# Performance work log

Measured on AMD Instinct MI355X. Metric: run time of the kernel, lower is better.

## Reference

```python
import jax, jax.numpy as jnp
import numpy as np

B, S, D = 2, 2048, 1024
H = 16
DK = D // H  # 64

def setup_inputs() -> dict:
    key = jax.random.key(0)
    ks = jax.random.split(key, 7)
    scale = 1.0 / np.sqrt(D)
    return {
        "Query": jax.random.normal(ks[0], (B, S, D), dtype=jnp.float32),
        "Key":   jax.random.normal(ks[1], (B, S, D), dtype=jnp.float32),
        "Value": jax.random.normal(ks[2], (B, S, D), dtype=jnp.float32),
        "Wq": jax.random.normal(ks[3], (D, D), dtype=jnp.float32) * scale,
        "Wk": jax.random.normal(ks[4], (D, D), dtype=jnp.float32) * scale,
        "Wv": jax.random.normal(ks[5], (D, D), dtype=jnp.float32) * scale,
        "Wo": jax.random.normal(ks[6], (D, D), dtype=jnp.float32) * scale,
    }

def reference(Query, Key, Value, Wq, Wk, Wv, Wo):
    b = Query.shape[0]
    # nn.Linear(bias=False): x @ W.T ; reshape to [B, H, S, DK]
    q = (Query @ Wq.T).reshape(b, -1, H, DK).transpose(0, 2, 1, 3)
    k = (Key   @ Wk.T).reshape(b, -1, H, DK).transpose(0, 2, 1, 3)
    v = (Value @ Wv.T).reshape(b, -1, H, DK).transpose(0, 2, 1, 3)
    # full O(S^2) score matrix [B, H, Sq, Sk]
    scores = jnp.einsum("bhqd,bhkd->bhqk", q, k) / jnp.sqrt(jnp.float32(DK))
    # FAITHFUL to source: nn.Softmax(dim=1) normalizes over the HEAD axis
    attn = jax.nn.softmax(scores, axis=1)
    ctx = jnp.einsum("bhqk,bhkd->bhqd", attn, v)  # [B, H, Sq, DK]
    ctx = ctx.transpose(0, 2, 1, 3).reshape(b, -1, H * DK)  # [B, S, D]
    return ctx @ Wo.T
```

## Files before the change

### kernel.cpp

```cpp
#include <hip/hip_runtime.h>
#include <stdint.h>

#define BB   2
#define SS   2048
#define DD   1024
#define HH   16
#define DKK  64
#define MM   (BB*SS)

typedef __attribute__((ext_vector_type(4))) float f32x4;
typedef __attribute__((ext_vector_type(8))) short s16x8;

#define MFMA_B16(a, b, c) __builtin_amdgcn_mfma_f32_16x16x32_bf16((a), (b), (c), 0, 0, 0)

__device__ __forceinline__ ushort f2bf(float f) {
  uint u = __float_as_uint(f);
  u += 0x7FFFu + ((u >> 16) & 1u);
  return (ushort)(u >> 16);
}
__device__ __forceinline__ float bf2f(ushort u) {
  return __uint_as_float((uint)u << 16);
}
#if __has_builtin(__builtin_amdgcn_exp2f)
#define EXP2(x) __builtin_amdgcn_exp2f(x)
#else
#define EXP2(x) exp2f(x)
#endif

__device__ __forceinline__ s16x8 pack8(float4 a, float4 b) {
  union { uint u[4]; s16x8 v; } r;
  asm("v_cvt_pk_bf16_f32 %0, %1, %2" : "=v"(r.u[0]) : "v"(a.x), "v"(a.y));
  asm("v_cvt_pk_bf16_f32 %0, %1, %2" : "=v"(r.u[1]) : "v"(a.z), "v"(a.w));
  asm("v_cvt_pk_bf16_f32 %0, %1, %2" : "=v"(r.u[2]) : "v"(b.x), "v"(b.y));
  asm("v_cvt_pk_bf16_f32 %0, %1, %2" : "=v"(r.u[3]) : "v"(b.z), "v"(b.w));
  return r.v;
}
__device__ __forceinline__ s16x8 cvt8(const float* src) {
  return pack8(*(const float4*)src, *(const float4*)(src + 4));
}

#define QSCALE (0.125f * 1.4426950408889634f)

__global__ void cvt4_kernel(const float* __restrict__ s0, const float* __restrict__ s1,
                            const float* __restrict__ s2, const float* __restrict__ s3,
                            ushort* __restrict__ d0, ushort* __restrict__ d1,
                            ushort* __restrict__ d2, ushort* __restrict__ d3, int n) {
  const int w = blockIdx.y;
  const float*  src = (w == 0) ? s0 : (w == 1) ? s1 : (w == 2) ? s2 : s3;
  ushort*       dst = (w == 0) ? d0 : (w == 1) ? d1 : (w == 2) ? d2 : d3;
  int i = (blockIdx.x * 256 + threadIdx.x) * 8;
  if (i >= n) return;
  *(s16x8*)(dst + i) = cvt8(src + i);
}

__global__ __launch_bounds__(256, 2) void qkv_proj(
    const float* __restrict__ Ia, const float* __restrict__ Ib, const float* __restrict__ Ic,
    const ushort* __restrict__ Wa, const ushort* __restrict__ Wb, const ushort* __restrict__ Wc,
    ushort* __restrict__ Oa, ushort* __restrict__ Ob, ushort* __restrict__ Oc)
{
  __shared__ ushort As[2][128 * 32];
  __shared__ ushort Bs[2][128 * 32];
  const int tid  = threadIdx.x;
  const int lane = tid & 63, wave = tid >> 6;
  const int q = lane & 15, g = lane >> 4;
  const int wr = wave >> 1, wc = wave & 1;
  const int mblk = blockIdx.x * 128, nblk = blockIdx.y * 128;
  const int mode = blockIdx.z;

  const float*  A = (mode == 0) ? Ia : (mode == 1) ? Ib : Ic;
  const ushort* W = (mode == 0) ? Wa : (mode == 1) ? Wb : Wc;

  f32x4 acc[4][4];
  {
    f32x4 z = {0.f, 0.f, 0.f, 0.f};
#pragma unroll
    for (int i = 0; i < 4; ++i)
#pragma unroll
      for (int j = 0; j < 4; ++j) acc[i][j] = z;
  }

  const int r0 = tid >> 2;
  const int e0 = (tid & 3) * 8;
  const size_t arow0 = (size_t)(mblk + r0) * 1024 + e0;
  const size_t arow1 = (size_t)(mblk + r0 + 64) * 1024 + e0;
  const size_t wrow0 = (size_t)(nblk + r0) * 1024 + e0;
  const size_t wrow1 = (size_t)(nblk + r0 + 64) * 1024 + e0;

#pragma unroll
  for (int it = 0; it < 2; ++it) {
    const int row = r0 + it * 64;
    *(s16x8*)&As[0][row * 32 + e0] = cvt8(A + (it ? arow1 : arow0));
    *(s16x8*)&Bs[0][row * 32 + e0] = *(const s16x8*)(W + (it ? wrow1 : wrow0));
  }
  float4 fa0_0, fa0_1, fa1_0, fa1_1;
  s16x8  wg0, wg1;
  {
    const float* p0 = A + arow0 + 32;
    const float* p1 = A + arow1 + 32;
    fa0_0 = *(const float4*)p0;  fa0_1 = *(const float4*)(p0 + 4);
    fa1_0 = *(const float4*)p1;  fa1_1 = *(const float4*)(p1 + 4);
    wg0 = *(const s16x8*)(W + wrow0 + 32);
    wg1 = *(const s16x8*)(W + wrow1 + 32);
  }
  __syncthreads();

  for (int s = 0; s < 32; ++s) {
    const int cur = s & 1;
    float4 na0_0, na0_1, na1_0, na1_1;
    s16x8  nw0, nw1;
    if (s < 30) {
      const int k0 = (s + 2) * 32;
      const float* p0 = A + arow0 + k0;
      const float* p1 = A + arow1 + k0;
      na0_0 = *(const float4*)p0;  na0_1 = *(const float4*)(p0 + 4);
      na1_0 = *(const float4*)p1;  na1_1 = *(const float4*)(p1 + 4);
      nw0 = *(const s16x8*)(W + wrow0 + k0);
      nw1 = *(const s16x8*)(W + wrow1 + k0);
    }
    s16x8 af[4], bf[4];
#pragma unroll
    for (int t = 0; t < 4; ++t) {
      af[t] = *(const s16x8*)&As[cur][(wr * 64 + t * 16 + q) * 32 + g * 8];
      bf[t] = *(const s16x8*)&Bs[cur][(wc * 64 + t * 16 + q) * 32 + g * 8];
    }
#pragma unroll
    for (int mt = 0; mt < 4; ++mt)
#pragma unroll
      for (int nt = 0; nt < 4; ++nt)
        acc[mt][nt] = MFMA_B16(af[mt], bf[nt], acc[mt][nt]);
    if (s < 31) {
      *(s16x8*)&As[cur ^ 1][r0 * 32 + e0]        = pack8(fa0_0, fa0_1);
      *(s16x8*)&As[cur ^ 1][(r0 + 64) * 32 + e0] = pack8(fa1_0, fa1_1);
      *(s16x8*)&Bs[cur ^ 1][r0 * 32 + e0]        = wg0;
      *(s16x8*)&Bs[cur ^ 1][(r0 + 64) * 32 + e0] = wg1;
    }
    if (s < 30) {
      fa0_0 = na0_0; fa0_1 = na0_1; fa1_0 = na1_0; fa1_1 = na1_1;
      wg0 = nw0; wg1 = nw1;
    }
    __syncthreads();
  }

  if (mode == 2) {
    ushort* Vt = Oc;
#pragma unroll
    for (int mt = 0; mt < 4; ++mt)
#pragma unroll
      for (int nt = 0; nt < 4; ++nt) {
        const int s0 = mblk + wr * 64 + mt * 16 + g * 4;
        const int o  = nblk + wc * 64 + nt * 16 + q;
        const int h = o >> 6, dk = o & 63;
        const int b = s0 >> 11, sr = s0 & 2047;
        ushort4 pk;
        pk.x = f2bf(acc[mt][nt][0]); pk.y = f2bf(acc[mt][nt][1]);
        pk.z = f2bf(acc[mt][nt][2]); pk.w = f2bf(acc[mt][nt][3]);
        *(ushort4*)(Vt + ((size_t)((b * 16 + h) * 64 + dk)) * SS + sr) = pk;
      }
  } else {
    const float scale = (mode == 0) ? QSCALE : 1.0f;
    ushort* P = (mode == 0) ? Oa : Ob;
    ushort* wl = &As[0][wave * 1024];
    const int h0 = (nblk + wc * 64) >> 6;
#pragma unroll
    for (int mt = 0; mt < 4; ++mt) {
      const int s0 = mblk + wr * 64 + mt * 16;
      const int b  = s0 >> 11, sr0 = s0 & 2047;
#pragma unroll
      for (int nt = 0; nt < 4; ++nt)
#pragma unroll
        for (int j = 0; j < 4; ++j)
          wl[(g * 4 + j) * 64 + nt * 16 + q] = f2bf(acc[mt][nt][j] * scale);
#pragma unroll
      for (int it = 0; it < 2; ++it) {
        s16x8 v = *(const s16x8*)((char*)wl + it * 1024 + lane * 16);
        const int lr = it * 8 + (lane >> 3);
        const int c  = (lane & 7) * 8;
        *(s16x8*)(P + ((size_t)((b * 16 + h0) * SS) + sr0 + lr) * DKK + c) = v;
      }
    }
  }
}

__global__ __launch_bounds__(256, 2) void o_proj(
    const ushort* __restrict__ A, const ushort* __restrict__ W,
    float* __restrict__ O)
{
  __shared__ ushort As[2][128 * 32];
  __shared__ ushort Bs[2][128 * 32];
  const int tid  = threadIdx.x;
  const int lane = tid & 63, wave = tid >> 6;
  const int q = lane & 15, g = lane >> 4;
  const int wr = wave >> 1, wc = wave & 1;
  const int mblk = blockIdx.x * 128, nblk = blockIdx.y * 128;

  f32x4 acc[4][4];
  {
    f32x4 z = {0.f, 0.f, 0.f, 0.f};
#pragma unroll
    for (int i = 0; i < 4; ++i)
#pragma unroll
      for (int j = 0; j < 4; ++j) acc[i][j] = z;
  }

  const int r0 = tid >> 2;
  const int e0 = (tid & 3) * 8;
  const size_t arow0 = (size_t)(mblk + r0) * 1024 + e0;
  const size_t arow1 = (size_t)(mblk + r0 + 64) * 1024 + e0;
  const size_t wrow0 = (size_t)(nblk + r0) * 1024 + e0;
  const size_t wrow1 = (size_t)(nblk + r0 + 64) * 1024 + e0;

#pragma unroll
  for (int it = 0; it < 2; ++it) {
    const int row = r0 + it * 64;
    *(s16x8*)&As[0][row * 32 + e0] = *(const s16x8*)(A + (it ? arow1 : arow0));
    *(s16x8*)&Bs[0][row * 32 + e0] = *(const s16x8*)(W + (it ? wrow1 : wrow0));
  }
  s16x8 ag0, ag1, wg0, wg1;
  {
    ag0 = *(const s16x8*)(A + arow0 + 32);
    ag1 = *(const s16x8*)(A + arow1 + 32);
    wg0 = *(const s16x8*)(W + wrow0 + 32);
    wg1 = *(const s16x8*)(W + wrow1 + 32);
  }
  __syncthreads();

  for (int s = 0; s < 32; ++s) {
    const int cur = s & 1;
    s16x8 na0, na1, nw0, nw1;
    if (s < 30) {
      const int k0 = (s + 2) * 32;
      na0 = *(const s16x8*)(A + arow0 + k0);
      na1 = *(const s16x8*)(A + arow1 + k0);
      nw0 = *(const s16x8*)(W + wrow0 + k0);
      nw1 = *(const s16x8*)(W + wrow1 + k0);
    }
    s16x8 af[4], bf[4];
#pragma unroll
    for (int t = 0; t < 4; ++t) {
      af[t] = *(const s16x8*)&As[cur][(wr * 64 + t * 16 + q) * 32 + g * 8];
      bf[t] = *(const s16x8*)&Bs[cur][(wc * 64 + t * 16 + q) * 32 + g * 8];
    }
#pragma unroll
    for (int mt = 0; mt < 4; ++mt)
#pragma unroll
      for (int nt = 0; nt < 4; ++nt)
        acc[mt][nt] = MFMA_B16(af[mt], bf[nt], acc[mt][nt]);
    if (s < 31) {
      *(s16x8*)&As[cur ^ 1][r0 * 32 + e0]        = ag0;
      *(s16x8*)&As[cur ^ 1][(r0 + 64) * 32 + e0] = ag1;
      *(s16x8*)&Bs[cur ^ 1][r0 * 32 + e0]        = wg0;
      *(s16x8*)&Bs[cur ^ 1][(r0 + 64) * 32 + e0] = wg1;
    }
    if (s < 30) { ag0 = na0; ag1 = na1; wg0 = nw0; wg1 = nw1; }
    __syncthreads();
  }

#pragma unroll
  for (int mt = 0; mt < 4; ++mt)
#pragma unroll
    for (int nt = 0; nt < 4; ++nt)
#pragma unroll
      for (int j = 0; j < 4; ++j) {
        const int s = mblk + wr * 64 + mt * 16 + g * 4 + j;
        const int o = nblk + wc * 64 + nt * 16 + q;
        O[(size_t)s * DD + o] = acc[mt][nt][j];
      }
}

__global__ __launch_bounds__(256, 2) void den_kernel(
    const ushort* __restrict__ Qp, const ushort* __restrict__ Kp,
    ushort* __restrict__ Rden)
{
  __shared__ ushort smem[2][16384];
  const int tid  = threadIdx.x;
  const int lane = tid & 63, wave = tid >> 6;
  const int q = lane & 15, g = lane >> 4;
  const int wr = wave >> 1, wc = wave & 1;
  const int kblk = blockIdx.x * 128, qblk = blockIdx.y * 128;
  const int b = blockIdx.z;

  f32x4 den[4][4];
  {
    f32x4 z = {0.f, 0.f, 0.f, 0.f};
#pragma unroll
    for (int i = 0; i < 4; ++i)
#pragma unroll
      for (int j = 0; j < 4; ++j) den[i][j] = z;
  }

  const int srow = tid >> 3, sseg = tid & 7;
  const int sd   = (sseg * 8) ^ ((srow & 7) << 3);

  const ushort* Kb0 = Kp + ((size_t)(b * 16) * SS + kblk) * DKK;
  const ushort* Qb0 = Qp + ((size_t)(b * 16) * SS + qblk) * DKK;

#pragma unroll
  for (int i = 0; i < 4; ++i) {
    const int row = srow + i * 32;
    *(s16x8*)&smem[0][row * 64 + sd]        = *(const s16x8*)(Kb0 + (size_t)row * DKK + sseg * 8);
    *(s16x8*)&smem[0][8192 + row * 64 + sd] = *(const s16x8*)(Qb0 + (size_t)row * DKK + sseg * 8);
  }
  __syncthreads();

  for (int s = 0; s < 16; ++s) {
    const int cur = s & 1;
    s16x8 nA[4], nB[4];
    if (s < 15) {
      const ushort* Kh = Kb0 + (size_t)(s + 1) * SS * DKK;
      const ushort* Qh = Qb0 + (size_t)(s + 1) * SS * DKK;
#pragma unroll
      for (int i = 0; i < 4; ++i) {
        const int row = srow + i * 32;
        nA[i] = *(const s16x8*)(Kh + (size_t)row * DKK + sseg * 8);
        nB[i] = *(const s16x8*)(Qh + (size_t)row * DKK + sseg * 8);
      }
    }
    s16x8 af[4][2], bf[4][2];
#pragma unroll
    for (int t = 0; t < 4; ++t) {
      const int ra = wr * 64 + t * 16 + q;
      const int rb = wc * 64 + t * 16 + q;
      af[t][0] = *(const s16x8*)&smem[cur][ra * 64 + ((g * 8) ^ ((ra & 7) << 3))];
      af[t][1] = *(const s16x8*)&smem[cur][ra * 64 + ((32 + g * 8) ^ ((ra & 7) << 3))];
      bf[t][0] = *(const s16x8*)&smem[cur][8192 + rb * 64 + ((g * 8) ^ ((rb & 7) << 3))];
      bf[t][1] = *(const s16x8*)&smem[cur][8192 + rb * 64 + ((32 + g * 8) ^ ((rb & 7) << 3))];
    }
#pragma unroll
    for (int mt = 0; mt < 4; ++mt)
#pragma unroll
      for (int nt = 0; nt < 4; ++nt) {
        f32x4 c = {0.f, 0.f, 0.f, 0.f};
        c = MFMA_B16(af[mt][0], bf[nt][0], c);
        c = MFMA_B16(af[mt][1], bf[nt][1], c);
#pragma unroll
        for (int r = 0; r < 4; ++r)
          den[mt][nt][r] += EXP2(c[r]);
      }
    if (s < 15) {
#pragma unroll
      for (int i = 0; i < 4; ++i) {
        const int row = srow + i * 32;
        *(s16x8*)&smem[cur ^ 1][row * 64 + sd]        = nA[i];
        *(s16x8*)&smem[cur ^ 1][8192 + row * 64 + sd] = nB[i];
      }
    }
    __syncthreads();
  }

  char* aw2 = (char*)smem + wave * 8192;
#pragma unroll
  for (int mt = 0; mt < 4; ++mt)
#pragma unroll
    for (int nt = 0; nt < 4; ++nt) {
      const int ql = nt * 16 + q;
      const float i0 = 1.0f / den[mt][nt][0], i1 = 1.0f / den[mt][nt][1];
      const float i2 = 1.0f / den[mt][nt][2], i3 = 1.0f / den[mt][nt][3];
      uint2 pk;
      asm("v_cvt_pk_bf16_f32 %0, %1, %2" : "=v"(pk.x) : "v"(i0), "v"(i1));
      asm("v_cvt_pk_bf16_f32 %0, %1, %2" : "=v"(pk.y) : "v"(i2), "v"(i3));
      *(uint2*)(aw2 + ql * 128 + ((mt * 32 + g * 8) ^ ((ql & 7) << 4))) = pk;
    }
#pragma unroll
  for (int it = 0; it < 8; ++it) {
    const int idx = it * 64 + lane;
    const int row = idx >> 3;
    const int seg = idx & 7;
    s16x8 v = *(const s16x8*)(aw2 + row * 128 + ((seg * 16) ^ ((row & 7) << 4)));
    *(s16x8*)(Rden + (size_t)b * SS * SS
              + (size_t)(qblk + wc * 64 + row) * SS
              + kblk + wr * 64 + seg * 8) = v;
  }
}

__global__ __launch_bounds__(512, 2) void attn5_kernel(
    const ushort* __restrict__ Qp, const ushort* __restrict__ Kp,
    const ushort* __restrict__ Vt, const ushort* __restrict__ Rden,
    ushort* __restrict__ Ctx)
{
  __shared__ ushort Ktile[2][64 * 64];
  __shared__ ushort Vtile[2][64 * 64];
  __shared__ ushort Rw_all[8][16 * 64];
  __shared__ ushort aw_all[8][16 * 64];

  const int tid  = threadIdx.x;
  const int lane = tid & 63;
  const int w    = tid >> 6;
  const int q    = lane & 15;
  const int g    = lane >> 4;
  const int bid  = blockIdx.x;
  const int bh   = bid & 31;
  const int b    = bh >> 4, h = bh & 15;
  const int qblk = (bid >> 5) * 128;

  const ushort* Qb = Qp + ((size_t)bh * SS + qblk + w * 16 + q) * DKK + g * 8;
  s16x8 qf0 = *(const s16x8*)(Qb);
  s16x8 qf1 = *(const s16x8*)(Qb + 32);

  const ushort* Ks = Kp + (size_t)bh * SS * DKK;
  const ushort* Vs = Vt + (size_t)bh * DKK * SS;
  const ushort* Rs = Rden + (size_t)b * SS * SS + (size_t)(qblk + w * 16) * SS;

  f32x4 acc[4];
  {
    f32x4 z = {0.f, 0.f, 0.f, 0.f};
#pragma unroll
    for (int n = 0; n < 4; ++n) acc[n] = z;
  }

  ushort* Rw = Rw_all[w];
  ushort* aw = aw_all[w];
  const int srow = tid >> 3, sseg = tid & 7;
  const int sd   = (sseg * 8) ^ ((srow & 7) << 3);
  const int r16  = lane >> 2;
  const int sgA  = (lane & 3) * 2;
  const int rd0  = r16 * 64 + ((sgA * 8) ^ ((r16 & 7) << 3));
  const int rd1  = r16 * 64 + (((sgA + 1) * 8) ^ ((r16 & 7) << 3));

  {
    s16x8 gK  = *(const s16x8*)(Ks + tid * 8);
    s16x8 gV  = *(const s16x8*)(Vs + (size_t)srow * SS + sseg * 8);
    s16x8 gR0 = *(const s16x8*)(Rs + (size_t)r16 * SS + sgA * 8);
    s16x8 gR1 = *(const s16x8*)(Rs + (size_t)r16 * SS + (sgA + 1) * 8);
    *(s16x8*)&Ktile[0][srow * 64 + sd] = gK;
    *(s16x8*)&Vtile[0][srow * 64 + sd] = gV;
    *(s16x8*)&Rw[rd0] = gR0;
    *(s16x8*)&Rw[rd1] = gR1;
  }
  __syncthreads();

  for (int kt = 0; kt < 32; ++kt) {
    const int cur = kt & 1;
    s16x8 gK, gV, gR0, gR1;
    if (kt < 31) {
      const int k1 = (kt + 1) * 64;
      gK  = *(const s16x8*)(Ks + (size_t)k1 * DKK + tid * 8);
      gV  = *(const s16x8*)(Vs + (size_t)srow * SS + k1 + sseg * 8);
      gR0 = *(const s16x8*)(Rs + (size_t)r16 * SS + k1 + sgA * 8);
      gR1 = *(const s16x8*)(Rs + (size_t)r16 * SS + k1 + (sgA + 1) * 8);
    }
    const ushort* Kt = Ktile[cur];
    const ushort* Vv = Vtile[cur];

#pragma unroll
    for (int ks = 0; ks < 4; ++ks) {
      const int kr = ks * 16 + q;
      s16x8 a0 = *(const s16x8*)&Kt[kr * 64 + ((g * 8) ^ ((kr & 7) << 3))];
      s16x8 a1 = *(const s16x8*)&Kt[kr * 64 + ((32 + g * 8) ^ ((kr & 7) << 3))];
      f32x4 c = {0.f, 0.f, 0.f, 0.f};
      c = MFMA_B16(a0, qf0, c);
      c = MFMA_B16(a1, qf1, c);
      ushort4 rv = *(const ushort4*)&Rw[q * 64 + (((ks * 2 + (g >> 1)) ^ (q & 7)) * 8) + (g & 1) * 4];
      float p0 = EXP2(c[0]) * bf2f(rv.x);
      float p1 = EXP2(c[1]) * bf2f(rv.y);
      float p2 = EXP2(c[2]) * bf2f(rv.z);
      float p3 = EXP2(c[3]) * bf2f(rv.w);
      uint2 pp;
      asm("v_cvt_pk_bf16_f32 %0, %1, %2" : "=v"(pp.x) : "v"(p0), "v"(p1));
      asm("v_cvt_pk_bf16_f32 %0, %1, %2" : "=v"(pp.y) : "v"(p2), "v"(p3));
      *(uint2*)&aw[q * 64 + ((ks * 16 + g * 4) ^ ((q & 7) << 3))] = pp;
    }
#pragma unroll
    for (int kc = 0; kc < 2; ++kc) {
      s16x8 vf[4];
#pragma unroll
      for (int n = 0; n < 4; ++n) {
        const int vr = n * 16 + q;
        vf[n] = *(const s16x8*)&Vv[vr * 64 + ((kc * 32 + g * 8) ^ ((vr & 7) << 3))];
      }
      s16x8 pa = *(const s16x8*)&aw[q * 64 + ((kc * 32 + g * 8) ^ ((q & 7) << 3))];
#pragma unroll
      for (int n = 0; n < 4; ++n)
        acc[n] = MFMA_B16(pa, vf[n], acc[n]);
    }
    if (kt < 31) {
      *(s16x8*)&Ktile[cur ^ 1][srow * 64 + sd] = gK;
      *(s16x8*)&Vtile[cur ^ 1][srow * 64 + sd] = gV;
      *(s16x8*)&Rw[rd0] = gR0;
      *(s16x8*)&Rw[rd1] = gR1;
    }
    __syncthreads();
  }

#pragma unroll
  for (int n = 0; n < 4; ++n)
#pragma unroll
    for (int j = 0; j < 4; ++j)
      aw[(g * 4 + j) * 64 + n * 16 + q] = f2bf(acc[n][j]);
  ushort* P = Ctx + ((size_t)(b * SS) + qblk + w * 16) * DD + h * 64;
#pragma unroll
  for (int it = 0; it < 2; ++it) {
    const int idx = it * 64 + lane;
    const int row = idx >> 3;
    const int seg = idx & 7;
    s16x8 v = *(const s16x8*)&aw[row * 64 + seg * 8];
    *(s16x8*)(P + (size_t)row * DD + seg * 8) = v;
  }
}

extern "C" void kernel_launch(void* const* d_in, const int* in_sizes, int n_in,
                              void* d_out, int out_size, void* d_ws, size_t ws_size,
                              hipStream_t stream) {
  const float* Query = (const float*)d_in[0];
  const float* Key   = (const float*)d_in[1];
  const float* Value = (const float*)d_in[2];
  const float* Wq    = (const float*)d_in[3];
  const float* Wk    = (const float*)d_in[4];
  const float* Wv    = (const float*)d_in[5];
  const float* Wo    = (const float*)d_in[6];

  size_t off = 0;
  char* ws = (char*)d_ws;
  auto alloc = [&](size_t bytes) -> void* {
    void* p = ws + off;
    off += (bytes + 255) & ~(size_t)255;
    return p;
  };
  const size_t nX = (size_t)MM * DD;
  const size_t nW = (size_t)DD * DD;
  const size_t nS = (size_t)BB * SS * SS;
  ushort* Wqb  = (ushort*)alloc(nW * 2);
  ushort* Wkb  = (ushort*)alloc(nW * 2);
  ushort* Wvb  = (ushort*)alloc(nW * 2);
  ushort* Wob  = (ushort*)alloc(nW * 2);
  ushort* Qp   = (ushort*)alloc(nX * 2);
  ushort* Kp   = (ushort*)alloc(nX * 2);
  ushort* Vtb  = (ushort*)alloc(nX * 2);
  ushort* Rden = (ushort*)alloc(nS * 2);
  ushort* Ctx  = (ushort*)alloc(nX * 2);

  cvt4_kernel<<<dim3((int)(nW / 2048), 4), 256, 0, stream>>>(
      Wq, Wk, Wv, Wo, Wqb, Wkb, Wvb, Wob, (int)nW);

  qkv_proj<<<dim3(32, 8, 3), 256, 0, stream>>>(
      Query, Key, Value, Wqb, Wkb, Wvb, Qp, Kp, Vtb);

  den_kernel<<<dim3(16, 16, 2), 256, 0, stream>>>(Qp, Kp, Rden);
  attn5_kernel<<<512, 512, 0, stream>>>(Qp, Kp, Vtb, Rden, Ctx);

  o_proj<<<dim3(32, 8), 256, 0, stream>>>(Ctx, Wob, (float*)d_out);
}
```

Measured before the change: 147.6 us.

## Store reciprocal denominators in MFMA fragment order to skip LDS staging

```diff
diff --git a/kernel.cpp b/kernel.cpp
--- a/kernel.cpp
+++ b/kernel.cpp
@@ -10,6 +10,8 @@
 
 typedef __attribute__((ext_vector_type(4))) float f32x4;
 typedef __attribute__((ext_vector_type(8))) short s16x8;
+
+union RdU { ushort u[8]; s16x8 v; };
 
 #define MFMA_B16(a, b, c) __builtin_amdgcn_mfma_f32_16x16x32_bf16((a), (b), (c), 0, 0, 0)
 
@@ -347,28 +349,19 @@
     __syncthreads();
   }
 
-  char* aw2 = (char*)smem + wave * 8192;
-#pragma unroll
-  for (int mt = 0; mt < 4; ++mt)
-#pragma unroll
-    for (int nt = 0; nt < 4; ++nt) {
-      const int ql = nt * 16 + q;
+  ushort* R2 = Rden + (((size_t)(b * 16 + blockIdx.y) * 32) + (blockIdx.x * 2 + wr)) * 8192;
+#pragma unroll
+  for (int nt = 0; nt < 4; ++nt) {
+    const int tid_t = (wc * 4 + nt) * 64 + g * 16 + q;
+#pragma unroll
+    for (int mt = 0; mt < 4; ++mt) {
       const float i0 = 1.0f / den[mt][nt][0], i1 = 1.0f / den[mt][nt][1];
       const float i2 = 1.0f / den[mt][nt][2], i3 = 1.0f / den[mt][nt][3];
-      uint2 pk;
-      asm("v_cvt_pk_bf16_f32 %0, %1, %2" : "=v"(pk.x) : "v"(i0), "v"(i1));
-      asm("v_cvt_pk_bf16_f32 %0, %1, %2" : "=v"(pk.y) : "v"(i2), "v"(i3));
-      *(uint2*)(aw2 + ql * 128 + ((mt * 32 + g * 8) ^ ((ql & 7) << 4))) = pk;
-    }
-#pragma unroll
-  for (int it = 0; it < 8; ++it) {
-    const int idx = it * 64 + lane;
-    const int row = idx >> 3;
-    const int seg = idx & 7;
-    s16x8 v = *(const s16x8*)(aw2 + row * 128 + ((seg * 16) ^ ((row & 7) << 4)));
-    *(s16x8*)(Rden + (size_t)b * SS * SS
-              + (size_t)(qblk + wc * 64 + row) * SS
-              + kblk + wr * 64 + seg * 8) = v;
+      union { ushort4 s; uint2 u; } pk;
+      asm("v_cvt_pk_bf16_f32 %0, %1, %2" : "=v"(pk.u.x) : "v"(i0), "v"(i1));
+      asm("v_cvt_pk_bf16_f32 %0, %1, %2" : "=v"(pk.u.y) : "v"(i2), "v"(i3));
+      *(ushort4*)(R2 + tid_t * 16 + mt * 4) = pk.s;
+    }
   }
 }
 
@@ -379,7 +372,6 @@
 {
   __shared__ ushort Ktile[2][64 * 64];
   __shared__ ushort Vtile[2][64 * 64];
-  __shared__ ushort Rw_all[8][16 * 64];
   __shared__ ushort aw_all[8][16 * 64];
 
   const int tid  = threadIdx.x;
@@ -390,7 +382,8 @@
   const int bid  = blockIdx.x;
   const int bh   = bid & 31;
   const int b    = bh >> 4, h = bh & 15;
-  const int qblk = (bid >> 5) * 128;
+  const int qt   = bid >> 5;
+  const int qblk = qt * 128;
 
   const ushort* Qb = Qp + ((size_t)bh * SS + qblk + w * 16 + q) * DKK + g * 8;
   s16x8 qf0 = *(const s16x8*)(Qb);
@@ -398,7 +391,7 @@
 
   const ushort* Ks = Kp + (size_t)bh * SS * DKK;
   const ushort* Vs = Vt + (size_t)bh * DKK * SS;
-  const ushort* Rs = Rden + (size_t)b * SS * SS + (size_t)(qblk + w * 16) * SS;
+  const ushort* Rs = Rden + ((size_t)(b * 16 + qt) * 32) * 8192 + tid * 16;
 
   f32x4 acc[4];
   {
@@ -407,36 +400,31 @@
     for (int n = 0; n < 4; ++n) acc[n] = z;
   }
 
-  ushort* Rw = Rw_all[w];
   ushort* aw = aw_all[w];
   const int srow = tid >> 3, sseg = tid & 7;
   const int sd   = (sseg * 8) ^ ((srow & 7) << 3);
-  const int r16  = lane >> 2;
-  const int sgA  = (lane & 3) * 2;
-  const int rd0  = r16 * 64 + ((sgA * 8) ^ ((r16 & 7) << 3));
-  const int rd1  = r16 * 64 + (((sgA + 1) * 8) ^ ((r16 & 7) << 3));
-
+
+  RdU rdA, rdB;
   {
     s16x8 gK  = *(const s16x8*)(Ks + tid * 8);
     s16x8 gV  = *(const s16x8*)(Vs + (size_t)srow * SS + sseg * 8);
-    s16x8 gR0 = *(const s16x8*)(Rs + (size_t)r16 * SS + sgA * 8);
-    s16x8 gR1 = *(const s16x8*)(Rs + (size_t)r16 * SS + (sgA + 1) * 8);
+    rdA.v = *(const s16x8*)(Rs);
+    rdB.v = *(const s16x8*)(Rs + 8);
     *(s16x8*)&Ktile[0][srow * 64 + sd] = gK;
     *(s16x8*)&Vtile[0][srow * 64 + sd] = gV;
-    *(s16x8*)&Rw[rd0] = gR0;
-    *(s16x8*)&Rw[rd1] = gR1;
   }
   __syncthreads();
 
   for (int kt = 0; kt < 32; ++kt) {
     const int cur = kt & 1;
-    s16x8 gK, gV, gR0, gR1;
+    s16x8 gK, gV;
+    RdU nrA, nrB;
     if (kt < 31) {
       const int k1 = (kt + 1) * 64;
       gK  = *(const s16x8*)(Ks + (size_t)k1 * DKK + tid * 8);
       gV  = *(const s16x8*)(Vs + (size_t)srow * SS + k1 + sseg * 8);
-      gR0 = *(const s16x8*)(Rs + (size_t)r16 * SS + k1 + sgA * 8);
-      gR1 = *(const s16x8*)(Rs + (size_t)r16 * SS + k1 + (sgA + 1) * 8);
+      nrA.v = *(const s16x8*)(Rs + (size_t)(kt + 1) * 8192);
+      nrB.v = *(const s16x8*)(Rs + (size_t)(kt + 1) * 8192 + 8);
     }
     const ushort* Kt = Ktile[cur];
     const ushort* Vv = Vtile[cur];
@@ -449,11 +437,12 @@
       f32x4 c = {0.f, 0.f, 0.f, 0.f};
       c = MFMA_B16(a0, qf0, c);
       c = MFMA_B16(a1, qf1, c);
-      ushort4 rv = *(const ushort4*)&Rw[q * 64 + (((ks * 2 + (g >> 1)) ^ (q & 7)) * 8) + (g & 1) * 4];
-      float p0 = EXP2(c[0]) * bf2f(rv.x);
-      float p1 = EXP2(c[1]) * bf2f(rv.y);
-      float p2 = EXP2(c[2]) * bf2f(rv.z);
-      float p3 = EXP2(c[3]) * bf2f(rv.w);
+      const ushort* ru = (ks < 2) ? rdA.u : rdB.u;
+      const int o4 = (ks & 1) * 4;
+      float p0 = EXP2(c[0]) * bf2f(ru[o4 + 0]);
+      float p1 = EXP2(c[1]) * bf2f(ru[o4 + 1]);
+      float p2 = EXP2(c[2]) * bf2f(ru[o4 + 2]);
+      float p3 = EXP2(c[3]) * bf2f(ru[o4 + 3]);
       uint2 pp;
       asm("v_cvt_pk_bf16_f32 %0, %1, %2" : "=v"(pp.x) : "v"(p0), "v"(p1));
       asm("v_cvt_pk_bf16_f32 %0, %1, %2" : "=v"(pp.y) : "v"(p2), "v"(p3));
@@ -475,8 +464,7 @@
     if (kt < 31) {
       *(s16x8*)&Ktile[cur ^ 1][srow * 64 + sd] = gK;
       *(s16x8*)&Vtile[cur ^ 1][srow * 64 + sd] = gV;
-      *(s16x8*)&Rw[rd0] = gR0;
-      *(s16x8*)&Rw[rd1] = gR1;
+      rdA = nrA; rdB = nrB;
     }
     __syncthreads();
   }
```

Measured after the change: 143.6 us, median of 3. 2.8% less time.
